# Optimization experiments

Measured on AMD Instinct MI355X. Metric: run time of the kernel, lower is better.

Reference implementation:

```python
import jax, jax.numpy as jnp
import numpy as np

B, S, F_IN, H, P2 = 64, 64, 2048, 512, 20  # batch, seq_len, input_size, hidden, 2*num_prototype


def setup_inputs() -> dict:
    key = jax.random.key(0)
    ks = jax.random.split(key, 16)
    sc = 0.02
    inp = {
        "v_feat": jax.random.normal(ks[0], (B, S, F_IN), jnp.float32),
        "category": jax.random.randint(ks[1], (B,), 0, 3, jnp.int64),
        "W_enc": jax.random.normal(ks[2], (F_IN, H), jnp.float32) * sc,
        "b_enc": jnp.zeros((H,), jnp.float32),
        # gate order along last axis: input, forget, output, memory(g)
        "Wx": jax.random.normal(ks[3], (H, 4 * H), jnp.float32) * sc,
        "bx": jnp.zeros((4 * H,), jnp.float32),
        "Wh": jax.random.normal(ks[4], (H, 4 * H), jnp.float32) * sc,
        "bh": jnp.zeros((4 * H,), jnp.float32),
        "cat_emb": jax.random.normal(ks[5], (3, H), jnp.float32) * sc,
        "W_dec": jax.random.normal(ks[6], (H, 1), jnp.float32) * sc,
        "b_dec": jnp.zeros((1,), jnp.float32),
        "prototype": jax.random.uniform(ks[7], (P2, F_IN), jnp.float32),
        "W_dd": jax.random.normal(ks[8], (P2 * S, 1), jnp.float32) * sc,
        "b_dd": jnp.zeros((1,), jnp.float32),
        "W_gate": jax.random.normal(ks[9], (F_IN, 1), jnp.float32) * sc,
        "b_gate": jnp.zeros((1,), jnp.float32),
    }
    return inp


def _forward(v_feat, category, W_enc, b_enc, Wx, bx, Wh, bh, cat_emb,
             W_dec, b_dec, prototype, W_dd, b_dd, W_gate, b_gate):
    batch, seq, feat = v_feat.shape
    # encoder + category fusion
    fuse = jax.nn.relu(jnp.einsum('bsf,fh->bsh', v_feat, W_enc) + b_enc)
    fuse = fuse + cat_emb[category][:, None, :]

    # fused-gate LSTM over time (note: original cell has NO tanh on cell in h = o*c)
    x_gates = jnp.einsum('bsh,hg->sbg', fuse, Wx) + (bx + bh)  # precompute input GEMM

    def step(carry, xg):
        h, c = carry
        gates = xg + h @ Wh
        i, f, o, g = jnp.split(gates, 4, axis=-1)
        i, f, o = jax.nn.sigmoid(i), jax.nn.sigmoid(f), jax.nn.sigmoid(o)
        g = jnp.tanh(g)
        c = f * c + i * g
        h = o * c
        return (h, c), None

    h0 = jnp.zeros((batch, Wh.shape[0]), fuse.dtype)
    (h, c), _ = jax.lax.scan(step, (h0, h0), x_gates)

    # dropout p=0.5 omitted (deterministic eval reference)
    output = jax.nn.sigmoid(h @ W_dec + b_dec)  # [B,1]

    # prototype distances: [B,S,2P]
    diff = v_feat[:, :, None, :] - prototype[None, None, :, :]
    dist = jnp.sum(diff * diff, axis=-1)
    dist_feat = jnp.log((dist + 1.0) / (dist + 1e-8))
    dist_pred = jax.nn.sigmoid(dist_feat.reshape(batch, -1) @ W_dd + b_dd)
    gate = jax.nn.sigmoid(jnp.mean(v_feat, axis=1) @ W_gate + b_gate)
    return output * gate + dist_pred * (1.0 - gate)


def reference(v_feat, category, W_enc, b_enc, Wx, bx, Wh, bh, cat_emb,
              W_dec, b_dec, prototype, W_dd, b_dd, W_gate, b_gate):
    return _forward(v_feat, category, W_enc, b_enc, Wx, bx, Wh, bh, cat_emb,
                    W_dec, b_dec, prototype, W_dd, b_dd, W_gate, b_gate)
```

## Files before the change

kernel.cpp:

```cpp
#include <hip/hip_runtime.h>
#include <cstdint>
#include <cstddef>


typedef __attribute__((ext_vector_type(8))) short short8;
typedef __attribute__((ext_vector_type(4))) float f32x4;
typedef unsigned long long ull;

__device__ __forceinline__ ushort f2bf(float x) {
    uint32_t u = __float_as_uint(x);
    return (ushort)((u + 0x7FFF + ((u >> 16) & 1)) >> 16);
}
__device__ __forceinline__ float bf2f(ushort u) {
    return __uint_as_float(((uint32_t)u) << 16);
}
__device__ __forceinline__ float sigm(float x) { return 1.f / (1.f + expf(-x)); }
__device__ __forceinline__ float tanh_fast(float x) { return 2.f / (1.f + expf(-2.f * x)) - 1.f; }

__global__ __launch_bounds__(256) void k_prep(
    const float* __restrict__ v_feat, const float* __restrict__ proto,
    const float* __restrict__ bx, const float* __restrict__ bh,
    const float* __restrict__ W_enc, const float* __restrict__ Wx,
    const float* __restrict__ Wh, const float* __restrict__ W_gate,
    ushort* __restrict__ v_bf16, ushort* __restrict__ proto_bf,
    float* __restrict__ bxh, ushort* __restrict__ Wenc_t,
    ushort* __restrict__ Wx_t, ushort* __restrict__ Whr,
    float* __restrict__ n2, float* __restrict__ gpart, float* __restrict__ p2,
    ushort* __restrict__ hbuf, int* __restrict__ flags, int* __restrict__ dd_done)
{
    __shared__ float ts[32][33];
    const int blk = blockIdx.x;
    const int tid = threadIdx.x;

    if (blk < 8192) {
        int i = blk * 256 + tid;
        float4 v = ((const float4*)v_feat)[i];
        ushort4 o;
        o.x = f2bf(v.x); o.y = f2bf(v.y); o.z = f2bf(v.z); o.w = f2bf(v.w);
        ((ushort4*)v_bf16)[i] = o;
    } else if (blk < 8232) {
        int i = (blk - 8192) * 256 + tid;
        float4 v = ((const float4*)proto)[i];
        ushort4 o;
        o.x = f2bf(v.x); o.y = f2bf(v.y); o.z = f2bf(v.z); o.w = f2bf(v.w);
        ((ushort4*)proto_bf)[i] = o;
    } else if (blk < 8244) {
        int row = 20 + (blk - 8232);
        ushort4 z = {0, 0, 0, 0};
        ((ushort4*)(proto_bf + (size_t)row * 2048))[tid * 2] = z;
        ((ushort4*)(proto_bf + (size_t)row * 2048))[tid * 2 + 1] = z;
    } else if (blk < 8252) {
        int n = (blk - 8244) * 256 + tid;
        int np = ((n & 511) << 2) | (n >> 9);
        bxh[np] = bx[n] + bh[n];
    } else if (blk < 11324) {
        const float* in;
        ushort* outp;
        int R, C, remap, t;
        if (blk < 9276)       { in = W_enc; outp = Wenc_t; R = 2048; C = 512;  remap = 0; t = blk - 8252; }
        else if (blk < 10300) { in = Wx;    outp = Wx_t;   R = 512;  C = 2048; remap = 1; t = blk - 9276; }
        else                  { in = Wh;    outp = Whr;    R = 512;  C = 2048; remap = 1; t = blk - 10300; }
        int tpr = C / 32;
        int cx = t % tpr, cy = t / tpr;
        int r0 = cy * 32, c0 = cx * 32;
        int rr = tid >> 3, cc = (tid & 7) * 4;
        float4 v = *(const float4*)(in + (size_t)(r0 + rr) * C + c0 + cc);
        ts[rr][cc + 0] = v.x; ts[rr][cc + 1] = v.y; ts[rr][cc + 2] = v.z; ts[rr][cc + 3] = v.w;
        __syncthreads();
        ushort4 o;
        o.x = f2bf(ts[cc + 0][rr]);
        o.y = f2bf(ts[cc + 1][rr]);
        o.z = f2bf(ts[cc + 2][rr]);
        o.w = f2bf(ts[cc + 3][rr]);
        int n = c0 + rr;
        int np = remap ? (((n & 511) << 2) | (n >> 9)) : n;
        *(ushort4*)(outp + (size_t)np * R + r0 + cc) = o;
    } else if (blk < 12348) {
        const int lane = tid & 63, w = tid >> 6;
        const int bs = (blk - 11324) * 4 + w;
        const float* vr = v_feat + (size_t)bs * 2048;
        float a = 0.f, g = 0.f;
#pragma unroll
        for (int i = 0; i < 8; ++i) {
            float4 x = ((const float4*)vr)[i * 64 + lane];
            float4 wg = ((const float4*)W_gate)[i * 64 + lane];
            a += x.x * x.x + x.y * x.y + x.z * x.z + x.w * x.w;
            g += x.x * wg.x + x.y * wg.y + x.z * wg.z + x.w * wg.w;
        }
#pragma unroll
        for (int o = 32; o > 0; o >>= 1) { a += __shfl_down(a, o); g += __shfl_down(g, o); }
        if (lane == 0) {
            n2[bs] = a;
            gpart[bs] = g;
        }
    } else if (blk == 12348) {
        const int lane = tid & 63, w = tid >> 6;
        for (int p = w; p < 20; p += 4) {
            const float* pr = proto + (size_t)p * 2048;
            float a = 0.f;
#pragma unroll
            for (int i = 0; i < 8; ++i) {
                float4 x = ((const float4*)pr)[i * 64 + lane];
                a += x.x * x.x + x.y * x.y + x.z * x.z + x.w * x.w;
            }
#pragma unroll
            for (int o = 32; o > 0; o >>= 1) a += __shfl_down(a, o);
            if (lane == 0) p2[p] = a;
        }
        if (tid == 0) *dd_done = 0;
    } else if (blk < 12381) {
        ((ull*)hbuf)[(blk - 12349) * 256 + tid] = 0ULL;
    } else {
        for (int i = tid; i < 2048; i += 256) flags[i] = 0;
    }
}

__global__ __launch_bounds__(256) void k_gemm_mfma(
    const ushort* __restrict__ A, const ushort* __restrict__ Bt,
    int M, int N, int K,
    const float* __restrict__ bias0,
    const float* __restrict__ cat_emb, const int* __restrict__ category,
    void* __restrict__ Cout, int mode)
{
    __shared__ ushort As[128][40];
    __shared__ ushort Bs[128][40];
    const int tid = threadIdx.x;
    const int lane = tid & 63, w = tid >> 6;
    const int quad = lane >> 4, l16 = lane & 15;
    const int m0 = blockIdx.y * 128, n0 = blockIdx.x * 128;
    const int wm = (w & 1) * 64, wn = (w >> 1) * 64;

    f32x4 acc[4][4] = {};
    const int lr = tid >> 2;
    const int lc = (tid & 3) * 8;

    for (int k0 = 0; k0 < K; k0 += 32) {
        uint4 a0 = *(const uint4*)(A + (size_t)(m0 + lr) * K + k0 + lc);
        uint4 a1 = *(const uint4*)(A + (size_t)(m0 + 64 + lr) * K + k0 + lc);
        uint4 b0 = *(const uint4*)(Bt + (size_t)(n0 + lr) * K + k0 + lc);
        uint4 b1 = *(const uint4*)(Bt + (size_t)(n0 + 64 + lr) * K + k0 + lc);
        __syncthreads();
        *(uint4*)&As[lr][lc] = a0;
        *(uint4*)&As[64 + lr][lc] = a1;
        *(uint4*)&Bs[lr][lc] = b0;
        *(uint4*)&Bs[64 + lr][lc] = b1;
        __syncthreads();
        short8 af[4], bf[4];
#pragma unroll
        for (int i = 0; i < 4; ++i) af[i] = *(const short8*)&As[wm + i * 16 + l16][quad * 8];
#pragma unroll
        for (int j = 0; j < 4; ++j) bf[j] = *(const short8*)&Bs[wn + j * 16 + l16][quad * 8];
#pragma unroll
        for (int i = 0; i < 4; ++i)
#pragma unroll
            for (int j = 0; j < 4; ++j)
                acc[i][j] = __builtin_amdgcn_mfma_f32_16x16x32_bf16(af[i], bf[j], acc[i][j], 0, 0, 0);
    }

    if (mode == 0) {
        ushort* C = (ushort*)Cout;
#pragma unroll
        for (int i = 0; i < 4; ++i) {
            int mbase = m0 + wm + i * 16 + quad * 4;
#pragma unroll
            for (int r = 0; r < 4; ++r) {
                int m = mbase + r;
                const float* ce = cat_emb + category[m >> 6] * 512;
#pragma unroll
                for (int j = 0; j < 4; ++j) {
                    int n = n0 + wn + j * 16 + l16;
                    float v = fmaxf(acc[i][j][r] + bias0[n], 0.f) + ce[n];
                    C[(size_t)m * 512 + n] = f2bf(v);
                }
            }
        }
    } else {
        ushort* C = (ushort*)Cout;
        float bb[4];
#pragma unroll
        for (int j = 0; j < 4; ++j) bb[j] = bias0[n0 + wn + j * 16 + l16];
#pragma unroll
        for (int i = 0; i < 4; ++i) {
            int mbase = m0 + wm + i * 16 + quad * 4;
#pragma unroll
            for (int r = 0; r < 4; ++r) {
                int m = mbase + r;
                int s = m & 63, b = m >> 6;
                ushort* crow = C + ((size_t)(s * 64 + b)) * 2048;
#pragma unroll
                for (int j = 0; j < 4; ++j)
                    crow[n0 + wn + j * 16 + l16] = f2bf(acc[i][j][r] + bb[j]);
            }
        }
    }
}

__global__ __launch_bounds__(256) void k_dot(const ushort* __restrict__ v_bf,
                                             const ushort* __restrict__ proto_bf,
                                             float* __restrict__ dots)
{
    const int tid = threadIdx.x;
    const int lane = tid & 63, w = tid >> 6;
    const int quad = lane >> 4, l16 = lane & 15;
    const int r0 = blockIdx.x * 64 + w * 16;

    f32x4 acc[2] = {};
    const ushort* arow = v_bf + (size_t)(r0 + l16) * 2048 + quad * 8;
    const ushort* b0p = proto_bf + (size_t)l16 * 2048 + quad * 8;
    const ushort* b1p = proto_bf + (size_t)(16 + l16) * 2048 + quad * 8;
#pragma unroll 8
    for (int kk = 0; kk < 64; ++kk) {
        short8 af = *(const short8*)(arow + kk * 32);
        short8 bf0 = *(const short8*)(b0p + kk * 32);
        short8 bf1 = *(const short8*)(b1p + kk * 32);
        acc[0] = __builtin_amdgcn_mfma_f32_16x16x32_bf16(af, bf0, acc[0], 0, 0, 0);
        acc[1] = __builtin_amdgcn_mfma_f32_16x16x32_bf16(af, bf1, acc[1], 0, 0, 0);
    }
#pragma unroll
    for (int t = 0; t < 2; ++t)
#pragma unroll
        for (int r = 0; r < 4; ++r)
            dots[(size_t)(r0 + quad * 4 + r) * 32 + t * 16 + l16] = acc[t][r];
}

__global__ __launch_bounds__(512, 2) void k_lstm_persist(
    const ushort* __restrict__ xg,
    const ushort* __restrict__ Whr,
    ushort* __restrict__ hbuf,
    int* __restrict__ flags,
    const float* __restrict__ W_dec, const float* __restrict__ b_dec,
    const float* __restrict__ b_dd, const float* __restrict__ b_gate,
    const float* __restrict__ dots, const float* __restrict__ n2,
    const float* __restrict__ p2, const float* __restrict__ W_dd,
    const float* __restrict__ gpart,
    float* __restrict__ dd_logit, float* __restrict__ g_logit,
    int* __restrict__ dd_done,
    float* __restrict__ out)
{
    __shared__ __align__(16) ushort hin_s[16 * 520];
    __shared__ __align__(16) ushort hstage[512];
    __shared__ float fred[8][64];

    const int tid = threadIdx.x;
    const int lane = tid & 63, wv = tid >> 6;
    const int quad = lane >> 4, l16 = lane & 15;
    const int bn = blockIdx.x;

    if (bn >= 64) {
        const int b = bn - 64;
        if (tid < 64) {
            float gp = gpart[b * 64 + tid];
#pragma unroll
            for (int o = 32; o > 0; o >>= 1) gp += __shfl_down(gp, o);
            if (tid == 0)
                __hip_atomic_store(&g_logit[b], gp, __ATOMIC_RELAXED, __HIP_MEMORY_SCOPE_AGENT);
        }
        float acc = 0.f;
        for (int u = tid; u < 1280; u += 512) {
            int s = u / 20, p = u - s * 20;
            int bs = b * 64 + s;
            float d = n2[bs] - 2.f * dots[(size_t)bs * 32 + p] + p2[p];
            acc += logf((d + 1.0f) / (d + 1e-8f)) * W_dd[s * 20 + p];
        }
#pragma unroll
        for (int o = 32; o > 0; o >>= 1) acc += __shfl_down(acc, o);
        if (lane == 0) fred[wv][0] = acc;
        __syncthreads();
        if (tid == 0) {
            float t = 0.f;
#pragma unroll
            for (int p = 0; p < 8; ++p) t += fred[p][0];
            __hip_atomic_store(&dd_logit[b], t, __ATOMIC_RELAXED, __HIP_MEMORY_SCOPE_AGENT);
            __hip_atomic_fetch_add(dd_done, 1, __ATOMIC_RELEASE, __HIP_MEMORY_SCOPE_AGENT);
        }
        return;
    }

    const int i = bn & 15;
    const int j = bn >> 4;
    const int uloc = wv * 4 + quad;

    short8 wfrag[16];
#pragma unroll
    for (int kc = 0; kc < 16; ++kc)
        wfrag[kc] = *(const short8*)(Whr +
            (size_t)(i * 128 + wv * 16 + l16) * 512 + kc * 32 + quad * 8);

    float c = 0.f;

    for (int s = 0; s < 64; ++s) {
        const ushort* xp = xg + (size_t)(s * 64 + j * 16 + l16) * 2048
                              + i * 128 + wv * 16 + quad * 4;
        ushort4 xa = *(const ushort4*)xp;

        if (s > 0) {
            if (tid < 16) {
                const int* f = flags + (j * 16 + tid) * 32;
                while (__hip_atomic_load(f, __ATOMIC_RELAXED,
                                         __HIP_MEMORY_SCOPE_AGENT) < s) {}
            }
            __builtin_amdgcn_s_barrier();
            asm volatile("" ::: "memory");
        }
        const ushort* hin = hbuf + (size_t)s * 32768 + j * 8192;
        ushort* hout = hbuf + (size_t)(s + 1) * 32768 + j * 8192;

        {
            int r0 = wv * 2;
            __builtin_amdgcn_global_load_lds(
                (const __attribute__((address_space(1))) void*)(hin + (size_t)r0 * 512 + lane * 8),
                (__attribute__((address_space(3))) void*)(hin_s + r0 * 520),
                16, 0, 0);
            __builtin_amdgcn_global_load_lds(
                (const __attribute__((address_space(1))) void*)(hin + (size_t)(r0 + 1) * 512 + lane * 8),
                (__attribute__((address_space(3))) void*)(hin_s + (r0 + 1) * 520),
                16, 0, 0);
        }
        asm volatile("s_waitcnt vmcnt(0)" ::: "memory");
        __builtin_amdgcn_s_barrier();
        asm volatile("" ::: "memory");

        f32x4 aA = {bf2f(xa.x), bf2f(xa.y), bf2f(xa.z), bf2f(xa.w)};
        f32x4 aB = {};
#pragma unroll
        for (int kc = 0; kc < 16; kc += 2) {
            short8 h0 = *(const short8*)(hin_s + l16 * 520 + kc * 32 + quad * 8);
            short8 h1 = *(const short8*)(hin_s + l16 * 520 + (kc + 1) * 32 + quad * 8);
            aA = __builtin_amdgcn_mfma_f32_16x16x32_bf16(wfrag[kc], h0, aA, 0, 0, 0);
            aB = __builtin_amdgcn_mfma_f32_16x16x32_bf16(wfrag[kc + 1], h1, aB, 0, 0, 0);
        }

        float gi = sigm(aA[0] + aB[0]);
        float gf = sigm(aA[1] + aB[1]);
        float go = sigm(aA[2] + aB[2]);
        float gg = tanh_fast(aA[3] + aB[3]);
        c = gf * c + gi * gg;
        hstage[l16 * 32 + uloc] = f2bf(go * c);

        asm volatile("s_waitcnt lgkmcnt(0)" ::: "memory");
        __builtin_amdgcn_s_barrier();
        asm volatile("" ::: "memory");

        if (tid < 128) {
            int r = tid >> 3, ch = tid & 7;
            __hip_atomic_store((ull*)(hout + (size_t)r * 512 + i * 32) + ch,
                               ((const ull*)hstage)[tid],
                               __ATOMIC_RELAXED, __HIP_MEMORY_SCOPE_AGENT);
        }
        __syncthreads();
        if (tid == 0)
            __hip_atomic_store(&flags[bn * 32], s + 1, __ATOMIC_RELAXED,
                               __HIP_MEMORY_SCOPE_AGENT);
    }

    if (bn == 0) {
        if (tid < 64) {
            while (__hip_atomic_load(&flags[tid * 32], __ATOMIC_RELAXED,
                                     __HIP_MEMORY_SCOPE_AGENT) < 64) {}
        }
        __syncthreads();
        asm volatile("" ::: "memory");
        const ushort* hb64 = hbuf + (size_t)64 * 32768;
        int b = tid & 63, part = tid >> 6;
        const ushort* row = hb64 + (size_t)(b >> 4) * 8192 + (b & 15) * 512;
        float acc = 0.f;
#pragma unroll
        for (int g8 = 0; g8 < 8; ++g8) {
            const ushort* hp = row + part * 64 + g8 * 8;
            const float* wd = W_dec + part * 64 + g8 * 8;
#pragma unroll
            for (int half = 0; half < 2; ++half) {
                ull u = *(const ull*)(hp + half * 4);
                acc += bf2f((ushort)u) * wd[half * 4]
                     + bf2f((ushort)(u >> 16)) * wd[half * 4 + 1]
                     + bf2f((ushort)(u >> 32)) * wd[half * 4 + 2]
                     + bf2f((ushort)(u >> 48)) * wd[half * 4 + 3];
            }
        }
        fred[part][b] = acc;
        __syncthreads();
        if (tid == 0) {
            while (__hip_atomic_load(dd_done, __ATOMIC_RELAXED,
                                     __HIP_MEMORY_SCOPE_AGENT) < 64) {}
        }
        __syncthreads();
        asm volatile("" ::: "memory");
        if (tid < 64) {
            float a = 0.f;
#pragma unroll
            for (int p = 0; p < 8; ++p) a += fred[p][tid];
            float gl = __hip_atomic_load(&g_logit[tid], __ATOMIC_RELAXED,
                                         __HIP_MEMORY_SCOPE_AGENT);
            float dl = __hip_atomic_load(&dd_logit[tid], __ATOMIC_RELAXED,
                                         __HIP_MEMORY_SCOPE_AGENT);
            float output = sigm(a + b_dec[0]);
            float gate   = sigm(gl * (1.0f / 64.f) + b_gate[0]);
            float ddp    = sigm(dl + b_dd[0]);
            out[tid] = output * gate + ddp * (1.f - gate);
        }
    }
}

extern "C" void kernel_launch(void* const* d_in, const int* in_sizes, int n_in,
                              void* d_out, int out_size, void* d_ws, size_t ws_size,
                              hipStream_t stream) {
    const float* v_feat   = (const float*)d_in[0];
    const int*   category = (const int*)d_in[1];
    const float* W_enc    = (const float*)d_in[2];
    const float* b_enc    = (const float*)d_in[3];
    const float* Wx       = (const float*)d_in[4];
    const float* bx       = (const float*)d_in[5];
    const float* Wh       = (const float*)d_in[6];
    const float* bh       = (const float*)d_in[7];
    const float* cat_emb  = (const float*)d_in[8];
    const float* W_dec    = (const float*)d_in[9];
    const float* b_dec    = (const float*)d_in[10];
    const float* proto    = (const float*)d_in[11];
    const float* W_dd     = (const float*)d_in[12];
    const float* b_dd     = (const float*)d_in[13];
    const float* W_gate   = (const float*)d_in[14];
    const float* b_gate   = (const float*)d_in[15];
    float* out = (float*)d_out;

    char* ws = (char*)d_ws;
    ushort* xg       = (ushort*)(ws + 0);
    ushort* v_bf16   = (ushort*)(ws + 0);
    ushort* fuse     = (ushort*)(ws + 16777216);
    ushort* Whr      = (ushort*)(ws + 20971520);
    ushort* Wenc_t   = (ushort*)(ws + 23068672);
    ushort* Wx_t     = (ushort*)(ws + 25165824);
    ushort* proto_bf = (ushort*)(ws + 27262976);
    float*  dots     = (float*)(ws + 27394048);
    float*  n2       = (float*)(ws + 27918336);
    float*  gpart    = (float*)(ws + 27934720);
    float*  p2       = (float*)(ws + 27951104);
    int*    dd_done  = (int*)(ws + 27951232);
    float*  bxh      = (float*)(ws + 27951616);
    int*    flags    = (int*)(ws + 27959808);
    float*  dd_logit = (float*)(ws + 27967744);
    float*  g_logit  = (float*)(ws + 27968000);
    ushort* hbuf     = (ushort*)(ws + 27968256);

    k_prep<<<12382, 256, 0, stream>>>(v_feat, proto, bx, bh, W_enc, Wx, Wh, W_gate,
                                      v_bf16, proto_bf, bxh, Wenc_t, Wx_t, Whr,
                                      n2, gpart, p2, hbuf, flags, dd_done);

    k_gemm_mfma<<<dim3(4, 32), 256, 0, stream>>>(v_bf16, Wenc_t, 4096, 512, 2048,
                                                 b_enc, cat_emb, category, fuse, 0);

    k_dot<<<64, 256, 0, stream>>>(v_bf16, proto_bf, dots);

    k_gemm_mfma<<<dim3(16, 32), 256, 0, stream>>>(fuse, Wx_t, 4096, 2048, 512,
                                                  bxh, nullptr, nullptr, xg, 1);

    k_lstm_persist<<<128, 512, 0, stream>>>(xg, Whr, hbuf, flags,
                                            W_dec, b_dec, b_dd, b_gate,
                                            dots, n2, p2, W_dd, gpart,
                                            dd_logit, g_logit, dd_done, out);
}
```

Before: 260.1 us.

## Restructure LSTM h exchange layout with per-wave flag waits and double-buffered LDS

```diff
diff --git a/kernel.cpp b/kernel.cpp
--- a/kernel.cpp
+++ b/kernel.cpp
@@ -237,7 +237,7 @@
     int* __restrict__ dd_done,
     float* __restrict__ out)
 {
-    __shared__ __align__(16) ushort hin_s[16 * 520];
+    __shared__ __align__(16) ushort hin_s[2][16 * 512];
     __shared__ __align__(16) ushort hstage[512];
     __shared__ float fred[8][64];
 
@@ -286,6 +286,9 @@
         wfrag[kc] = *(const short8*)(Whr +
             (size_t)(i * 128 + wv * 16 + l16) * 512 + kc * 32 + quad * 8);
 
+    const int fA = (j * 16 + wv) * 32;
+    const int fB = (j * 16 + wv + 8) * 32;
+
     float c = 0.f;
 
     for (int s = 0; s < 64; ++s) {
@@ -293,29 +296,28 @@
                               + i * 128 + wv * 16 + quad * 4;
         ushort4 xa = *(const ushort4*)xp;
 
+        const ushort* hin = hbuf + (size_t)s * 32768 + j * 8192;
+        ushort* lds_h = hin_s[s & 1];
+
         if (s > 0) {
-            if (tid < 16) {
-                const int* f = flags + (j * 16 + tid) * 32;
-                while (__hip_atomic_load(f, __ATOMIC_RELAXED,
-                                         __HIP_MEMORY_SCOPE_AGENT) < s) {}
-            }
-            __builtin_amdgcn_s_barrier();
-            asm volatile("" ::: "memory");
-        }
-        const ushort* hin = hbuf + (size_t)s * 32768 + j * 8192;
-        ushort* hout = hbuf + (size_t)(s + 1) * 32768 + j * 8192;
-
-        {
-            int r0 = wv * 2;
-            __builtin_amdgcn_global_load_lds(
-                (const __attribute__((address_space(1))) void*)(hin + (size_t)r0 * 512 + lane * 8),
-                (__attribute__((address_space(3))) void*)(hin_s + r0 * 520),
-                16, 0, 0);
-            __builtin_amdgcn_global_load_lds(
-                (const __attribute__((address_space(1))) void*)(hin + (size_t)(r0 + 1) * 512 + lane * 8),
-                (__attribute__((address_space(3))) void*)(hin_s + (r0 + 1) * 520),
-                16, 0, 0);
-        }
+            const int* f = flags + fA;
+            while (__hip_atomic_load(f, __ATOMIC_RELAXED,
+                                     __HIP_MEMORY_SCOPE_AGENT) < s) {}
+        }
+        __builtin_amdgcn_global_load_lds(
+            (const __attribute__((address_space(1))) void*)(hin + (size_t)wv * 512 + lane * 8),
+            (__attribute__((address_space(3))) void*)(lds_h + wv * 512),
+            16, 0, 0);
+        if (s > 0) {
+            const int* f = flags + fB;
+            while (__hip_atomic_load(f, __ATOMIC_RELAXED,
+                                     __HIP_MEMORY_SCOPE_AGENT) < s) {}
+        }
+        __builtin_amdgcn_global_load_lds(
+            (const __attribute__((address_space(1))) void*)(hin + (size_t)(wv + 8) * 512 + lane * 8),
+            (__attribute__((address_space(3))) void*)(lds_h + (wv + 8) * 512),
+            16, 0, 0);
+
         asm volatile("s_waitcnt vmcnt(0)" ::: "memory");
         __builtin_amdgcn_s_barrier();
         asm volatile("" ::: "memory");
@@ -324,8 +326,8 @@
         f32x4 aB = {};
 #pragma unroll
         for (int kc = 0; kc < 16; kc += 2) {
-            short8 h0 = *(const short8*)(hin_s + l16 * 520 + kc * 32 + quad * 8);
-            short8 h1 = *(const short8*)(hin_s + l16 * 520 + (kc + 1) * 32 + quad * 8);
+            short8 h0 = *(const short8*)(lds_h + kc * 512 + l16 * 32 + quad * 8);
+            short8 h1 = *(const short8*)(lds_h + (kc + 1) * 512 + l16 * 32 + quad * 8);
             aA = __builtin_amdgcn_mfma_f32_16x16x32_bf16(wfrag[kc], h0, aA, 0, 0, 0);
             aB = __builtin_amdgcn_mfma_f32_16x16x32_bf16(wfrag[kc + 1], h1, aB, 0, 0, 0);
         }
@@ -341,16 +343,19 @@
         __builtin_amdgcn_s_barrier();
         asm volatile("" ::: "memory");
 
-        if (tid < 128) {
-            int r = tid >> 3, ch = tid & 7;
-            __hip_atomic_store((ull*)(hout + (size_t)r * 512 + i * 32) + ch,
-                               ((const ull*)hstage)[tid],
+        if (wv == 0) {
+            ushort* hout = hbuf + (size_t)(s + 1) * 32768 + j * 8192 + i * 512;
+            ull u0 = ((const ull*)hstage)[lane * 2];
+            ull u1 = ((const ull*)hstage)[lane * 2 + 1];
+            __hip_atomic_store((ull*)hout + lane * 2, u0,
                                __ATOMIC_RELAXED, __HIP_MEMORY_SCOPE_AGENT);
-        }
-        __syncthreads();
-        if (tid == 0)
-            __hip_atomic_store(&flags[bn * 32], s + 1, __ATOMIC_RELAXED,
-                               __HIP_MEMORY_SCOPE_AGENT);
+            __hip_atomic_store((ull*)hout + lane * 2 + 1, u1,
+                               __ATOMIC_RELAXED, __HIP_MEMORY_SCOPE_AGENT);
+            asm volatile("s_waitcnt vmcnt(0)" ::: "memory");
+            if (lane == 0)
+                __hip_atomic_store(&flags[bn * 32], s + 1, __ATOMIC_RELAXED,
+                                   __HIP_MEMORY_SCOPE_AGENT);
+        }
     }
 
     if (bn == 0) {
@@ -362,19 +367,20 @@
         asm volatile("" ::: "memory");
         const ushort* hb64 = hbuf + (size_t)64 * 32768;
         int b = tid & 63, part = tid >> 6;
-        const ushort* row = hb64 + (size_t)(b >> 4) * 8192 + (b & 15) * 512;
+        const ushort* base = hb64 + (size_t)(b >> 4) * 8192 + (b & 15) * 32;
         float acc = 0.f;
 #pragma unroll
-        for (int g8 = 0; g8 < 8; ++g8) {
-            const ushort* hp = row + part * 64 + g8 * 8;
-            const float* wd = W_dec + part * 64 + g8 * 8;
-#pragma unroll
-            for (int half = 0; half < 2; ++half) {
-                ull u = *(const ull*)(hp + half * 4);
-                acc += bf2f((ushort)u) * wd[half * 4]
-                     + bf2f((ushort)(u >> 16)) * wd[half * 4 + 1]
-                     + bf2f((ushort)(u >> 32)) * wd[half * 4 + 2]
-                     + bf2f((ushort)(u >> 48)) * wd[half * 4 + 3];
+        for (int sl = 0; sl < 2; ++sl) {
+            int isl = part * 2 + sl;
+            const ushort* hp = base + (size_t)isl * 512;
+            const float* wd = W_dec + isl * 32;
+#pragma unroll
+            for (int q = 0; q < 8; ++q) {
+                ull u = *(const ull*)(hp + q * 4);
+                acc += bf2f((ushort)u) * wd[q * 4]
+                     + bf2f((ushort)(u >> 16)) * wd[q * 4 + 1]
+                     + bf2f((ushort)(u >> 32)) * wd[q * 4 + 2]
+                     + bf2f((ushort)(u >> 48)) * wd[q * 4 + 3];
             }
         }
         fred[part][b] = acc;
```

Result: slower. 280.6 us (+7.9%).

## Merge encoder GEMM and prototype dot kernel into one launch with smaller tiles

Applied to the files above, without the earlier changes.

```diff
diff --git a/kernel.cpp b/kernel.cpp
--- a/kernel.cpp
+++ b/kernel.cpp
@@ -115,12 +115,93 @@
     }
 }
 
+__global__ __launch_bounds__(256) void k_mid(
+    const ushort* __restrict__ A, const ushort* __restrict__ Bt,
+    const float* __restrict__ bias0,
+    const float* __restrict__ cat_emb, const int* __restrict__ category,
+    ushort* __restrict__ C,
+    const ushort* __restrict__ proto_bf, float* __restrict__ dots)
+{
+    __shared__ ushort As[64][40];
+    __shared__ ushort Bs[128][40];
+    const int tid = threadIdx.x;
+    const int lane = tid & 63, w = tid >> 6;
+    const int quad = lane >> 4, l16 = lane & 15;
+    const int blk = blockIdx.x;
+
+    if (blk >= 256) {
+        const int r0 = (blk - 256) * 64 + w * 16;
+        f32x4 acc[2] = {};
+        const ushort* arow = A + (size_t)(r0 + l16) * 2048 + quad * 8;
+        const ushort* b0p = proto_bf + (size_t)l16 * 2048 + quad * 8;
+        const ushort* b1p = proto_bf + (size_t)(16 + l16) * 2048 + quad * 8;
+#pragma unroll 8
+        for (int kk = 0; kk < 64; ++kk) {
+            short8 af = *(const short8*)(arow + kk * 32);
+            short8 bf0 = *(const short8*)(b0p + kk * 32);
+            short8 bf1 = *(const short8*)(b1p + kk * 32);
+            acc[0] = __builtin_amdgcn_mfma_f32_16x16x32_bf16(af, bf0, acc[0], 0, 0, 0);
+            acc[1] = __builtin_amdgcn_mfma_f32_16x16x32_bf16(af, bf1, acc[1], 0, 0, 0);
+        }
+#pragma unroll
+        for (int t = 0; t < 2; ++t)
+#pragma unroll
+            for (int r = 0; r < 4; ++r)
+                dots[(size_t)(r0 + quad * 4 + r) * 32 + t * 16 + l16] = acc[t][r];
+        return;
+    }
+
+    const int m0 = (blk >> 2) * 64, n0 = (blk & 3) * 128;
+    const int wm = (w & 1) * 32, wn = (w >> 1) * 64;
+    const int K = 2048;
+
+    f32x4 acc[2][4] = {};
+    const int lr = tid >> 2;
+    const int lc = (tid & 3) * 8;
+
+    for (int k0 = 0; k0 < K; k0 += 32) {
+        uint4 a0 = *(const uint4*)(A + (size_t)(m0 + lr) * K + k0 + lc);
+        uint4 b0 = *(const uint4*)(Bt + (size_t)(n0 + lr) * K + k0 + lc);
+        uint4 b1 = *(const uint4*)(Bt + (size_t)(n0 + 64 + lr) * K + k0 + lc);
+        __syncthreads();
+        *(uint4*)&As[lr][lc] = a0;
+        *(uint4*)&Bs[lr][lc] = b0;
+        *(uint4*)&Bs[64 + lr][lc] = b1;
+        __syncthreads();
+        short8 af[2], bf[4];
+#pragma unroll
+        for (int i = 0; i < 2; ++i) af[i] = *(const short8*)&As[wm + i * 16 + l16][quad * 8];
+#pragma unroll
+        for (int j = 0; j < 4; ++j) bf[j] = *(const short8*)&Bs[wn + j * 16 + l16][quad * 8];
+#pragma unroll
+        for (int i = 0; i < 2; ++i)
+#pragma unroll
+            for (int j = 0; j < 4; ++j)
+                acc[i][j] = __builtin_amdgcn_mfma_f32_16x16x32_bf16(af[i], bf[j], acc[i][j], 0, 0, 0);
+    }
+
+#pragma unroll
+    for (int i = 0; i < 2; ++i) {
+        int mbase = m0 + wm + i * 16 + quad * 4;
+#pragma unroll
+        for (int r = 0; r < 4; ++r) {
+            int m = mbase + r;
+            const float* ce = cat_emb + category[m >> 6] * 512;
+#pragma unroll
+            for (int j = 0; j < 4; ++j) {
+                int n = n0 + wn + j * 16 + l16;
+                float v = fmaxf(acc[i][j][r] + bias0[n], 0.f) + ce[n];
+                C[(size_t)m * 512 + n] = f2bf(v);
+            }
+        }
+    }
+}
+
 __global__ __launch_bounds__(256) void k_gemm_mfma(
     const ushort* __restrict__ A, const ushort* __restrict__ Bt,
     int M, int N, int K,
     const float* __restrict__ bias0,
-    const float* __restrict__ cat_emb, const int* __restrict__ category,
-    void* __restrict__ Cout, int mode)
+    ushort* __restrict__ C)
 {
     __shared__ ushort As[128][40];
     __shared__ ushort Bs[128][40];
@@ -157,70 +238,22 @@
                 acc[i][j] = __builtin_amdgcn_mfma_f32_16x16x32_bf16(af[i], bf[j], acc[i][j], 0, 0, 0);
     }
 
-    if (mode == 0) {
-        ushort* C = (ushort*)Cout;
-#pragma unroll
-        for (int i = 0; i < 4; ++i) {
-            int mbase = m0 + wm + i * 16 + quad * 4;
-#pragma unroll
-            for (int r = 0; r < 4; ++r) {
-                int m = mbase + r;
-                const float* ce = cat_emb + category[m >> 6] * 512;
-#pragma unroll
-                for (int j = 0; j < 4; ++j) {
-                    int n = n0 + wn + j * 16 + l16;
-                    float v = fmaxf(acc[i][j][r] + bias0[n], 0.f) + ce[n];
-                    C[(size_t)m * 512 + n] = f2bf(v);
-                }
-            }
-        }
-    } else {
-        ushort* C = (ushort*)Cout;
-        float bb[4];
-#pragma unroll
-        for (int j = 0; j < 4; ++j) bb[j] = bias0[n0 + wn + j * 16 + l16];
-#pragma unroll
-        for (int i = 0; i < 4; ++i) {
-            int mbase = m0 + wm + i * 16 + quad * 4;
-#pragma unroll
-            for (int r = 0; r < 4; ++r) {
-                int m = mbase + r;
-                int s = m & 63, b = m >> 6;
-                ushort* crow = C + ((size_t)(s * 64 + b)) * 2048;
-#pragma unroll
-                for (int j = 0; j < 4; ++j)
-                    crow[n0 + wn + j * 16 + l16] = f2bf(acc[i][j][r] + bb[j]);
-            }
-        }
-    }
-}
-
-__global__ __launch_bounds__(256) void k_dot(const ushort* __restrict__ v_bf,
-                                             const ushort* __restrict__ proto_bf,
-                                             float* __restrict__ dots)
-{
-    const int tid = threadIdx.x;
-    const int lane = tid & 63, w = tid >> 6;
-    const int quad = lane >> 4, l16 = lane & 15;
-    const int r0 = blockIdx.x * 64 + w * 16;
-
-    f32x4 acc[2] = {};
-    const ushort* arow = v_bf + (size_t)(r0 + l16) * 2048 + quad * 8;
-    const ushort* b0p = proto_bf + (size_t)l16 * 2048 + quad * 8;
-    const ushort* b1p = proto_bf + (size_t)(16 + l16) * 2048 + quad * 8;
-#pragma unroll 8
-    for (int kk = 0; kk < 64; ++kk) {
-        short8 af = *(const short8*)(arow + kk * 32);
-        short8 bf0 = *(const short8*)(b0p + kk * 32);
-        short8 bf1 = *(const short8*)(b1p + kk * 32);
-        acc[0] = __builtin_amdgcn_mfma_f32_16x16x32_bf16(af, bf0, acc[0], 0, 0, 0);
-        acc[1] = __builtin_amdgcn_mfma_f32_16x16x32_bf16(af, bf1, acc[1], 0, 0, 0);
-    }
-#pragma unroll
-    for (int t = 0; t < 2; ++t)
-#pragma unroll
-        for (int r = 0; r < 4; ++r)
-            dots[(size_t)(r0 + quad * 4 + r) * 32 + t * 16 + l16] = acc[t][r];
+    float bb[4];
+#pragma unroll
+    for (int j = 0; j < 4; ++j) bb[j] = bias0[n0 + wn + j * 16 + l16];
+#pragma unroll
+    for (int i = 0; i < 4; ++i) {
+        int mbase = m0 + wm + i * 16 + quad * 4;
+#pragma unroll
+        for (int r = 0; r < 4; ++r) {
+            int m = mbase + r;
+            int s = m & 63, b = m >> 6;
+            ushort* crow = C + ((size_t)(s * 64 + b)) * 2048;
+#pragma unroll
+            for (int j = 0; j < 4; ++j)
+                crow[n0 + wn + j * 16 + l16] = f2bf(acc[i][j][r] + bb[j]);
+        }
+    }
 }
 
 __global__ __launch_bounds__(512, 2) void k_lstm_persist(
@@ -445,13 +478,11 @@
                                       v_bf16, proto_bf, bxh, Wenc_t, Wx_t, Whr,
                                       n2, gpart, p2, hbuf, flags, dd_done);
 
-    k_gemm_mfma<<<dim3(4, 32), 256, 0, stream>>>(v_bf16, Wenc_t, 4096, 512, 2048,
-                                                 b_enc, cat_emb, category, fuse, 0);
-
-    k_dot<<<64, 256, 0, stream>>>(v_bf16, proto_bf, dots);
+    k_mid<<<320, 256, 0, stream>>>(v_bf16, Wenc_t, b_enc, cat_emb, category,
+                                   fuse, proto_bf, dots);
 
     k_gemm_mfma<<<dim3(16, 32), 256, 0, stream>>>(fuse, Wx_t, 4096, 2048, 512,
-                                                  bxh, nullptr, nullptr, xg, 1);
+                                                  bxh, xg);
 
     k_lstm_persist<<<128, 512, 0, stream>>>(xg, Whr, hbuf, flags,
                                             W_dec, b_dec, b_dd, b_gate,
```

Result: faster. 235.6 us (-9.4%).
